# Kernel optimization log

Measured on AMD Instinct MI355X. Metric: run time of the kernel, lower is better.

The kernel has to match this reference:

```python
import jax, jax.numpy as jnp
import numpy as np

B, T, C = 1, 2048, 1024
H = 16
HD = C // H
BLOCK = 2048
NEG = float('-inf')

def setup_inputs() -> dict:
    key = jax.random.key(0)
    ks = jax.random.split(key, 6)
    x = jax.random.normal(ks[0], (B, T, C), dtype=jnp.float32)
    cumulative_scores = jax.random.normal(ks[1], (B, T), dtype=jnp.float32) * 0.1
    padding_mask = jnp.ones((B, T), dtype=jnp.float32)
    token_index = jax.random.randint(ks[2], (B, T), 0, BLOCK).astype(jnp.int64)
    w_attn = jax.random.normal(ks[3], (C, 3 * C), dtype=jnp.float32) * (1.0 / np.sqrt(C))
    b_attn = jnp.zeros((3 * C,), dtype=jnp.float32)
    w_proj = jax.random.normal(ks[4], (C, C), dtype=jnp.float32) * (1.0 / np.sqrt(C))
    b_proj = jnp.zeros((C,), dtype=jnp.float32)
    return dict(x=x, cumulative_scores=cumulative_scores, padding_mask=padding_mask,
                token_index=token_index, w_attn=w_attn, b_attn=b_attn,
                w_proj=w_proj, b_proj=b_proj)

def _rotate_half(z):
    z1, z2 = z[..., : z.shape[-1] // 2], z[..., z.shape[-1] // 2 :]
    return jnp.concatenate((-z2, z1), axis=-1)

def reference(x, cumulative_scores, padding_mask, token_index, w_attn, b_attn, w_proj, b_proj):
    # fused QKV projection
    qkv = x @ w_attn + b_attn                      # (B,T,3C)
    q, k, v = jnp.split(qkv, 3, axis=2)
    q = q.reshape(B, T, H, HD).transpose(0, 2, 1, 3)  # (B,H,T,HD)
    k = k.reshape(B, T, H, HD).transpose(0, 2, 1, 3)
    v = v.reshape(B, T, H, HD).transpose(0, 2, 1, 3)

    # dynamic per-token RoPE positions: global token counts (original scatter
    # broadcasts indices over batch, so counts are global across all batches)
    cnt = jnp.zeros((BLOCK,), jnp.float32).at[token_index.reshape(-1)].add(1.0)
    per_tok = (1.0 / (cnt + 1e-10))[token_index]       # (B,T)
    partial = jnp.cumsum(per_tok, axis=-1)             # (B,T) fractional positions

    inv_freq = 1.0 / (10000.0 ** (jnp.arange(0, HD, 2, dtype=jnp.float32) / HD))
    freqs = partial[..., None] * inv_freq              # (B,T,HD/2)
    emb = jnp.concatenate((freqs, freqs), axis=-1)     # (B,T,HD)
    cos = jnp.cos(emb)[:, None]                        # (B,1,T,HD)
    sin = jnp.sin(emb)[:, None]
    q = q * cos + _rotate_half(q) * sin
    k = k * cos + _rotate_half(k) * sin

    # 'fork' plan: overwrite last channel
    q = q.at[..., -1].set(1.0)
    k = k.at[..., -1].set(jnp.broadcast_to(cumulative_scores[:, None, :], (B, H, T)))

    # additive causal + padding mask (B,T,T)
    causal = jnp.where(jnp.tril(jnp.ones((T, T), jnp.bool_)), 0.0, NEG)
    pm = jnp.take_along_axis(padding_mask, token_index, axis=1)     # (B,T)
    outer = pm[:, :, None] * pm[:, None, :]
    pad_add = jnp.where(outer.astype(jnp.bool_), 0.0, NEG)
    mask = causal[None, :, :] + pad_add                              # (B,T,T)

    # scale v by exp(cumulative_scores)
    v = v * jnp.exp(cumulative_scores)[:, None, :, None]

    scores = jnp.einsum('bhqd,bhkd->bhqk', q, k) / np.sqrt(HD) + mask[:, None]
    probs = jax.nn.softmax(scores, axis=-1)
    y = jnp.einsum('bhqk,bhkd->bhqd', probs, v)        # (B,H,T,HD)
    y = y.transpose(0, 2, 1, 3).reshape(B, T, C)
    return y @ w_proj + b_proj
```

## Files before the change

kernel.cpp:

```cpp
#include <hip/hip_runtime.h>
#include <math.h>

#define T 2048
#define C 1024
#define H 16
#define HD 64
#define N3 (3*C)
#define NBLOCK 2048

typedef __attribute__((ext_vector_type(8))) short bf16x8;
typedef __attribute__((ext_vector_type(4))) float f32x4;

#define MFMA16(a, b, c) __builtin_amdgcn_mfma_f32_16x16x32_bf16((a), (b), (c), 0, 0, 0)

__device__ inline short f2bf(float f) {
    unsigned u; __builtin_memcpy(&u, &f, 4);
    unsigned r = (u + 0x7fffu + ((u >> 16) & 1u)) >> 16;
    return (short)r;
}
__device__ inline float bf2f(short s) {
    unsigned u = ((unsigned)(unsigned short)s) << 16;
    float f; __builtin_memcpy(&f, &u, 4);
    return f;
}

__device__ inline void gload_lds16(const void* g, void* l) {
    __builtin_amdgcn_global_load_lds((const __attribute__((address_space(1))) unsigned int*)g,
                                     (__attribute__((address_space(3))) unsigned int*)l,
                                     16, 0, 0);
}

__global__ __launch_bounds__(256) void pre_kernel(const float* __restrict__ x,
                                                  const float* __restrict__ w_attn,
                                                  const int* __restrict__ tok,
                                                  const float* __restrict__ padmask,
                                                  short* __restrict__ xb,
                                                  short* __restrict__ wabT,
                                                  float* __restrict__ partial,
                                                  float* __restrict__ pm_tok) {
    int bid = blockIdx.x;
    int tid = threadIdx.x;
    if (bid == 2816) {
        __shared__ float cntS[NBLOCK];
        __shared__ float sums[256];
        #pragma unroll
        for (int j = 0; j < 8; ++j) cntS[tid * 8 + j] = 0.0f;
        __syncthreads();
        int tk[8];
        #pragma unroll
        for (int j = 0; j < 8; ++j) {
            tk[j] = tok[tid * 8 + j];
            atomicAdd(&cntS[tk[j]], 1.0f);
        }
        __syncthreads();
        float vals[8];
        float s = 0.0f;
        #pragma unroll
        for (int j = 0; j < 8; ++j) {
            s += 1.0f / (cntS[tk[j]] + 1e-10f);
            vals[j] = s;
            pm_tok[tid * 8 + j] = padmask[tk[j]];
        }
        sums[tid] = s;
        __syncthreads();
        for (int off = 1; off < 256; off <<= 1) {
            float v = (tid >= off) ? sums[tid - off] : 0.0f;
            __syncthreads();
            sums[tid] += v;
            __syncthreads();
        }
        float offset = (tid > 0) ? sums[tid - 1] : 0.0f;
        #pragma unroll
        for (int j = 0; j < 8; ++j) partial[tid * 8 + j] = offset + vals[j];
        return;
    }
    if (bid < 2048) {
        int i = bid * 1024 + tid * 4;
        float4 v = *(const float4*)(x + i);
        short4 o;
        o.x = f2bf(v.x); o.y = f2bf(v.y); o.z = f2bf(v.z); o.w = f2bf(v.w);
        *(short4*)(xb + i) = o;
        return;
    }
    __shared__ float S[64][65];
    int b = bid - 2048;
    int bx = b % 48, by = b / 48;
    int n0 = bx * 64, k0 = by * 64;
    #pragma unroll
    for (int i = 0; i < 16; ++i) {
        int lin = tid + i * 256;
        int r = lin >> 6, c = lin & 63;
        S[r][c] = w_attn[(size_t)(k0 + r) * N3 + n0 + c];
    }
    __syncthreads();
    #pragma unroll
    for (int i = 0; i < 16; ++i) {
        int lin = tid + i * 256;
        int rn = lin >> 6, ck = lin & 63;
        wabT[(size_t)(n0 + rn) * C + k0 + ck] = f2bf(S[ck][rn]);
    }
}

template <int OUT_BF16, int EPI>
__global__ __launch_bounds__(256) void gemm_bt64(const short* __restrict__ A,
                                                 const short* __restrict__ Bt,
                                                 const float* __restrict__ bias,
                                                 void* __restrict__ Cout,
                                                 int M, int N, int K,
                                                 const float* __restrict__ partial,
                                                 const float* __restrict__ cumsc,
                                                 const float* __restrict__ pm_tok,
                                                 short* __restrict__ vbT) {
    __shared__ alignas(16) short As[64 * 32];
    __shared__ alignas(16) short Bs[128 * 32];
    int tid = threadIdx.x;
    int m0 = blockIdx.y * 64, n0 = blockIdx.x * 128;
    int w = tid >> 6, l = tid & 63;
    int wm = (w >> 1) * 32, wn = (w & 1) * 64;
    int lq = l & 15, g = l >> 4;
    int prow = l >> 2, pcol = (l & 3) * 8;
    f32x4 acc[2][4] = {};
    for (int k0 = 0; k0 < K; k0 += 32) {
        {
            int rowA = w * 16 + prow;
            gload_lds16(A + (size_t)(m0 + rowA) * K + k0 + pcol, As + w * 512);
            #pragma unroll
            for (int i = 0; i < 2; ++i) {
                int c = w * 2 + i;
                int row = c * 16 + prow;
                gload_lds16(Bt + (size_t)(n0 + row) * K + k0 + pcol, Bs + c * 512);
            }
        }
        __syncthreads();
        bf16x8 af[2], bfr[4];
        #pragma unroll
        for (int f = 0; f < 2; ++f)
            af[f] = *(const bf16x8*)(As + (wm + f * 16 + lq) * 32 + g * 8);
        #pragma unroll
        for (int j = 0; j < 4; ++j)
            bfr[j] = *(const bf16x8*)(Bs + (wn + j * 16 + lq) * 32 + g * 8);
        #pragma unroll
        for (int fi = 0; fi < 2; ++fi)
            #pragma unroll
            for (int fj = 0; fj < 4; ++fj)
                acc[fi][fj] = MFMA16(af[fi], bfr[fj], acc[fi][fj]);
        __syncthreads();
    }

    if (EPI == 0) {
        #pragma unroll
        for (int fi = 0; fi < 2; ++fi)
            #pragma unroll
            for (int fj = 0; fj < 4; ++fj)
                #pragma unroll
                for (int r = 0; r < 4; ++r) {
                    int m = m0 + wm + fi * 16 + g * 4 + r;
                    int n = n0 + wn + fj * 16 + lq;
                    float v = acc[fi][fj][r] + bias[n];
                    if (OUT_BF16) ((short*)Cout)[(size_t)m * N + n] = f2bf(v);
                    else          ((float*)Cout)[(size_t)m * N + n] = v;
                }
    } else {
        short* Cb = (short*)Cout;
        int cb = n0 + wn;
        int section = cb >> 10;
        float b0 = bias[cb + lq],      b1 = bias[cb + 16 + lq];
        float b2 = bias[cb + 32 + lq], b3 = bias[cb + 48 + lq];
        if (section < 2) {
            bool isQ = (section == 0);
            float inv0 = exp2f(-(float)lq * (13.287712379549449f / 32.0f));
            float inv1 = exp2f(-(float)(lq + 16) * (13.287712379549449f / 32.0f));
            #pragma unroll
            for (int fi = 0; fi < 2; ++fi)
                #pragma unroll
                for (int r = 0; r < 4; ++r) {
                    int trow = m0 + wm + fi * 16 + g * 4 + r;
                    float pt = partial[trow];
                    float sn0, cs0, sn1, cs1;
                    __sincosf(pt * inv0, &sn0, &cs0);
                    __sincosf(pt * inv1, &sn1, &cs1);
                    float a0 = acc[fi][0][r] + b0;
                    float a1 = acc[fi][1][r] + b1;
                    float a2 = acc[fi][2][r] + b2;
                    float a3 = acc[fi][3][r] + b3;
                    float lo0 = a0 * cs0 - a2 * sn0;
                    float hi0 = a2 * cs0 + a0 * sn0;
                    float lo1 = a1 * cs1 - a3 * sn1;
                    float hi1 = a3 * cs1 + a1 * sn1;
                    if (lq == 15) {
                        float pm = pm_tok[trow];
                        hi1 = isQ ? ((pm != 0.0f) ? 1.0f : 0.0f)
                                  : ((pm != 0.0f) ? cumsc[trow] : -1e20f);
                    }
                    size_t base = (size_t)trow * N3 + cb;
                    Cb[base + lq]      = f2bf(lo0);
                    Cb[base + 16 + lq] = f2bf(lo1);
                    Cb[base + 32 + lq] = f2bf(hi0);
                    Cb[base + 48 + lq] = f2bf(hi1);
                }
        } else {
            int h = (cb - 2 * C) >> 6;
            #pragma unroll
            for (int fi = 0; fi < 2; ++fi) {
                int tb = m0 + wm + fi * 16 + g * 4;
                float ef[4];
                #pragma unroll
                for (int r = 0; r < 4; ++r) ef[r] = __expf(cumsc[tb + r]);
                #pragma unroll
                for (int fj = 0; fj < 4; ++fj) {
                    int d = fj * 16 + lq;
                    float bv = (fj == 0) ? b0 : (fj == 1) ? b1 : (fj == 2) ? b2 : b3;
                    short4 o;
                    o.x = f2bf((acc[fi][fj][0] + bv) * ef[0]);
                    o.y = f2bf((acc[fi][fj][1] + bv) * ef[1]);
                    o.z = f2bf((acc[fi][fj][2] + bv) * ef[2]);
                    o.w = f2bf((acc[fi][fj][3] + bv) * ef[3]);
                    *(short4*)(vbT + (size_t)(h * 64 + d) * T + tb) = o;
                }
            }
        }
    }
}

__global__ __launch_bounds__(256) void attn_flash(const short* __restrict__ qkvb,
                                                  const short* __restrict__ vbT,
                                                  short* __restrict__ yb,
                                                  const float* __restrict__ w_proj,
                                                  short* __restrict__ wpbT) {
    __shared__ alignas(16) short Kt[2][64 * 64];
    __shared__ alignas(16) short Vt[2][64 * 64];
    __shared__ alignas(16) short Ps[4][16 * 64];

    int b = blockIdx.x;
    int tid = threadIdx.x;

    if (b >= 512) {
        int bb = b - 512;
        int bx = bb & 15, by = bb >> 4;
        int n0 = bx * 64, k0 = by * 64;
        short (*S)[72] = (short(*)[72])Kt;
        #pragma unroll
        for (int e = 0; e < 2; ++e) {
            int s = tid * 2 + e;
            int r = s >> 3, c8 = (s & 7) * 8;
            float4 v0 = *(const float4*)(w_proj + (size_t)(k0 + r) * C + n0 + c8);
            float4 v1 = *(const float4*)(w_proj + (size_t)(k0 + r) * C + n0 + c8 + 4);
            bf16x8 o;
            o[0] = f2bf(v0.x); o[1] = f2bf(v0.y); o[2] = f2bf(v0.z); o[3] = f2bf(v0.w);
            o[4] = f2bf(v1.x); o[5] = f2bf(v1.y); o[6] = f2bf(v1.z); o[7] = f2bf(v1.w);
            *(bf16x8*)&S[r][c8] = o;
        }
        __syncthreads();
        #pragma unroll
        for (int e = 0; e < 2; ++e) {
            int s = tid * 2 + e;
            int rn = s >> 3, k8 = (s & 7) * 8;
            bf16x8 o;
            #pragma unroll
            for (int i = 0; i < 8; ++i) o[i] = S[k8 + i][rn];
            *(bf16x8*)(wpbT + (size_t)(n0 + rn) * C + k0 + k8) = o;
        }
        return;
    }

    int h, qt;
    if (b < 256) { h = b & 15; qt = 31 - (b >> 4); }
    else         { int c2 = b - 256; h = c2 & 15; qt = c2 >> 4; }
    int w = tid >> 6, l = tid & 63;
    int lq = l & 15, g = l >> 4;
    int qrl = w * 16 + lq;
    char* psBase = (char*)Ps + w * 2048 + lq * 128;
    int psSw = (lq & 7) << 4;

    const short* qbase = qkvb + (size_t)(qt * 64 + qrl) * N3 + h * 64;
    bf16x8 qf0 = *(const bf16x8*)(qbase + g * 8);
    bf16x8 qf1 = *(const bf16x8*)(qbase + 32 + g * 8);

    f32x4 accO[4] = {};
    float lsum = 0.0f;

    int srow = tid >> 3, scol = (tid & 7) * 8;
    const short* kgb = qkvb + C + h * 64 + scol;
    const short* vgb = vbT + (size_t)(h * 64) * T + scol;
    int wb0 = srow * 128 + ((scol * 2) ^ ((srow & 7) << 4));
    int wb1 = (srow + 32) * 128 + ((scol * 2) ^ ((srow & 7) << 4));

    auto do_tile = [&](int cur, bool masked) {
        const char* Kc = (const char*)Kt[cur];
        const char* Vc = (const char*)Vt[cur];
        f32x4 s[4] = {};
        __builtin_amdgcn_s_setprio(1);
        #pragma unroll
        for (int f = 0; f < 4; ++f) {
            int row = f * 16 + lq;
            const char* kr_ = Kc + row * 128;
            int sw = (row & 7) << 4;
            bf16x8 a0 = *(const bf16x8*)(kr_ + ((g * 16) ^ sw));
            bf16x8 a1 = *(const bf16x8*)(kr_ + ((64 + g * 16) ^ sw));
            s[f] = MFMA16(a0, qf0, s[f]);
            s[f] = MFMA16(a1, qf1, s[f]);
        }
        __builtin_amdgcn_s_setprio(0);
        float p[16];
        #pragma unroll
        for (int f = 0; f < 4; ++f)
            #pragma unroll
            for (int r = 0; r < 4; ++r) {
                float sv = s[f][r] * 0.125f;
                if (masked) {
                    int kl = f * 16 + g * 4 + r;
                    sv = (kl > qrl) ? -INFINITY : sv;
                }
                float pv = __expf(sv);
                p[f * 4 + r] = pv;
                lsum += pv;
            }
        #pragma unroll
        for (int f = 0; f < 4; ++f) {
            unsigned u0, u1;
            asm("v_cvt_pk_bf16_f32 %0, %1, %2" : "=v"(u0) : "v"(p[f * 4 + 0]), "v"(p[f * 4 + 1]));
            asm("v_cvt_pk_bf16_f32 %0, %1, %2" : "=v"(u1) : "v"(p[f * 4 + 2]), "v"(p[f * 4 + 3]));
            uint2 uu; uu.x = u0; uu.y = u1;
            *(uint2*)(psBase + ((f * 32 + g * 8) ^ psSw)) = uu;
        }
        __builtin_amdgcn_s_setprio(1);
        #pragma unroll
        for (int kh = 0; kh < 2; ++kh) {
            bf16x8 pa = *(const bf16x8*)(psBase + ((kh * 64 + g * 16) ^ psSw));
            #pragma unroll
            for (int f = 0; f < 4; ++f) {
                int vrow = f * 16 + lq;
                const char* vr_ = Vc + vrow * 128;
                bf16x8 vb = *(const bf16x8*)(vr_ + (((kh * 32 + g * 8) * 2) ^ ((vrow & 7) << 4)));
                accO[f] = MFMA16(pa, vb, accO[f]);
            }
        }
        __builtin_amdgcn_s_setprio(0);
    };

    uint4 kr0 = *(const uint4*)(kgb + (size_t)srow * N3);
    uint4 kr1 = *(const uint4*)(kgb + (size_t)(srow + 32) * N3);
    uint4 vr0 = *(const uint4*)(vgb + (size_t)srow * T);
    uint4 vr1 = *(const uint4*)(vgb + (size_t)(srow + 32) * T);
    *(uint4*)((char*)Kt[0] + wb0) = kr0;
    *(uint4*)((char*)Kt[0] + wb1) = kr1;
    *(uint4*)((char*)Vt[0] + wb0) = vr0;
    *(uint4*)((char*)Vt[0] + wb1) = vr1;
    __syncthreads();

    for (int t = 0; t < qt; ++t) {
        int kn = (t + 1) * 64;
        kr0 = *(const uint4*)(kgb + (size_t)(kn + srow) * N3);
        kr1 = *(const uint4*)(kgb + (size_t)(kn + srow + 32) * N3);
        vr0 = *(const uint4*)(vgb + (size_t)srow * T + kn);
        vr1 = *(const uint4*)(vgb + (size_t)(srow + 32) * T + kn);

        do_tile(t & 1, false);

        int nxt = (t & 1) ^ 1;
        *(uint4*)((char*)Kt[nxt] + wb0) = kr0;
        *(uint4*)((char*)Kt[nxt] + wb1) = kr1;
        *(uint4*)((char*)Vt[nxt] + wb0) = vr0;
        *(uint4*)((char*)Vt[nxt] + wb1) = vr1;
        __syncthreads();
    }
    do_tile(qt & 1, true);

    lsum += __shfl_xor(lsum, 16);
    lsum += __shfl_xor(lsum, 32);
    float linv_own = 1.0f / lsum;
    float li[4];
    #pragma unroll
    for (int r = 0; r < 4; ++r) li[r] = __shfl(linv_own, g * 4 + r);

    #pragma unroll
    for (int f = 0; f < 4; ++f)
        #pragma unroll
        for (int r = 0; r < 4; ++r) {
            int trow = qt * 64 + w * 16 + g * 4 + r;
            yb[(size_t)trow * C + h * 64 + f * 16 + lq] = f2bf(accO[f][r] * li[r]);
        }
}

extern "C" void kernel_launch(void* const* d_in, const int* in_sizes, int n_in,
                              void* d_out, int out_size, void* d_ws, size_t ws_size,
                              hipStream_t stream) {
    const float* x       = (const float*)d_in[0];
    const float* cumsc   = (const float*)d_in[1];
    const float* padmask = (const float*)d_in[2];
    const int*   tok     = (const int*)d_in[3];
    const float* w_attn  = (const float*)d_in[4];
    const float* b_attn  = (const float*)d_in[5];
    const float* w_proj  = (const float*)d_in[6];
    const float* b_proj  = (const float*)d_in[7];
    float* out = (float*)d_out;

    float* part   = (float*)d_ws;
    float* pm_tok = part + 2048;
    short* xb     = (short*)(pm_tok + 2048);
    short* wabT   = xb + (size_t)T * C;
    short* wpbT   = wabT + (size_t)N3 * C;
    short* qkvb   = wpbT + (size_t)C * C;
    short* vbT    = qkvb + (size_t)T * N3;
    short* yb     = vbT + (size_t)C * T;

    pre_kernel<<<2817, 256, 0, stream>>>(x, w_attn, tok, padmask,
                                         xb, wabT, part, pm_tok);
    gemm_bt64<1, 1><<<dim3(N3 / 128, T / 64), 256, 0, stream>>>(
        xb, wabT, b_attn, qkvb, T, N3, C, part, cumsc, pm_tok, vbT);
    attn_flash<<<768, 256, 0, stream>>>(qkvb, vbT, yb, w_proj, wpbT);
    gemm_bt64<0, 0><<<dim3(C / 128, T / 64), 256, 0, stream>>>(
        yb, wpbT, b_proj, out, T, C, C, nullptr, nullptr, nullptr, nullptr);
}
```

Baseline: 88.71 us.

## Triple-buffer K/V tiles and software-pipeline QK with softmax-PV

Grows the K/V shared-memory ring from two to three buffers and prefetches two tiles ahead. Each iteration computes the QK scores for the next tile before doing softmax and PV on the current one. The goal is to let the MFMA work of the two stages interleave and to hide global-load latency better. In exchange it adds LDS use (16KB more per block), which may lower occupancy, and keeps an extra set of score registers live, raising register pressure.

Measured after the change: 90.25 us. Within noise of the previous version (+1.7%).

```diff
diff --git a/kernel.cpp b/kernel.cpp
--- a/kernel.cpp
+++ b/kernel.cpp
@@ -227,8 +227,8 @@
                                                   short* __restrict__ yb,
                                                   const float* __restrict__ w_proj,
                                                   short* __restrict__ wpbT) {
-    __shared__ alignas(16) short Kt[2][64 * 64];
-    __shared__ alignas(16) short Vt[2][64 * 64];
+    __shared__ alignas(16) short Kt[3][64 * 64];
+    __shared__ alignas(16) short Vt[3][64 * 64];
     __shared__ alignas(16) short Ps[4][16 * 64];
 
     int b = blockIdx.x;
@@ -285,10 +285,23 @@
     int wb0 = srow * 128 + ((scol * 2) ^ ((srow & 7) << 4));
     int wb1 = (srow + 32) * 128 + ((scol * 2) ^ ((srow & 7) << 4));
 
-    auto do_tile = [&](int cur, bool masked) {
-        const char* Kc = (const char*)Kt[cur];
-        const char* Vc = (const char*)Vt[cur];
-        f32x4 s[4] = {};
+    uint4 kr0, kr1, vr0, vr1;
+    auto stageRegs = [&](int tile) {
+        int kb = tile * 64;
+        kr0 = *(const uint4*)(kgb + (size_t)(kb + srow) * N3);
+        kr1 = *(const uint4*)(kgb + (size_t)(kb + srow + 32) * N3);
+        vr0 = *(const uint4*)(vgb + (size_t)srow * T + kb);
+        vr1 = *(const uint4*)(vgb + (size_t)(srow + 32) * T + kb);
+    };
+    auto writeLds = [&](int buf) {
+        *(uint4*)((char*)Kt[buf] + wb0) = kr0;
+        *(uint4*)((char*)Kt[buf] + wb1) = kr1;
+        *(uint4*)((char*)Vt[buf] + wb0) = vr0;
+        *(uint4*)((char*)Vt[buf] + wb1) = vr1;
+    };
+
+    auto computeQK = [&](int buf, f32x4* s) {
+        const char* Kc = (const char*)Kt[buf];
         __builtin_amdgcn_s_setprio(1);
         #pragma unroll
         for (int f = 0; f < 4; ++f) {
@@ -301,6 +314,10 @@
             s[f] = MFMA16(a1, qf1, s[f]);
         }
         __builtin_amdgcn_s_setprio(0);
+    };
+
+    auto softmaxPV = [&](int buf, f32x4* s, bool masked) {
+        const char* Vc = (const char*)Vt[buf];
         float p[16];
         #pragma unroll
         for (int f = 0; f < 4; ++f)
@@ -338,33 +355,27 @@
         __builtin_amdgcn_s_setprio(0);
     };
 
-    uint4 kr0 = *(const uint4*)(kgb + (size_t)srow * N3);
-    uint4 kr1 = *(const uint4*)(kgb + (size_t)(srow + 32) * N3);
-    uint4 vr0 = *(const uint4*)(vgb + (size_t)srow * T);
-    uint4 vr1 = *(const uint4*)(vgb + (size_t)(srow + 32) * T);
-    *(uint4*)((char*)Kt[0] + wb0) = kr0;
-    *(uint4*)((char*)Kt[0] + wb1) = kr1;
-    *(uint4*)((char*)Vt[0] + wb0) = vr0;
-    *(uint4*)((char*)Vt[0] + wb1) = vr1;
+    stageRegs(0);
+    writeLds(0);
+    if (qt >= 1) { stageRegs(1); writeLds(1); }
     __syncthreads();
 
+    f32x4 sC[4] = {};
+    computeQK(0, sC);
+
+    int bc = 0, bn = 1, bp = 2;
     for (int t = 0; t < qt; ++t) {
-        int kn = (t + 1) * 64;
-        kr0 = *(const uint4*)(kgb + (size_t)(kn + srow) * N3);
-        kr1 = *(const uint4*)(kgb + (size_t)(kn + srow + 32) * N3);
-        vr0 = *(const uint4*)(vgb + (size_t)srow * T + kn);
-        vr1 = *(const uint4*)(vgb + (size_t)(srow + 32) * T + kn);
-
-        do_tile(t & 1, false);
-
-        int nxt = (t & 1) ^ 1;
-        *(uint4*)((char*)Kt[nxt] + wb0) = kr0;
-        *(uint4*)((char*)Kt[nxt] + wb1) = kr1;
-        *(uint4*)((char*)Vt[nxt] + wb0) = vr0;
-        *(uint4*)((char*)Vt[nxt] + wb1) = vr1;
-        __syncthreads();
-    }
-    do_tile(qt & 1, true);
+        if (t + 2 <= qt) stageRegs(t + 2);
+        f32x4 sN[4] = {};
+        computeQK(bn, sN);
+        softmaxPV(bc, sC, false);
+        if (t + 2 <= qt) writeLds(bp);
+        __syncthreads();
+        #pragma unroll
+        for (int f = 0; f < 4; ++f) sC[f] = sN[f];
+        int tmp = bc; bc = bn; bn = bp; bp = tmp;
+    }
+    softmaxPV(bc, sC, true);
 
     lsum += __shfl_xor(lsum, 16);
     lsum += __shfl_xor(lsum, 32);
```
